# Optimization experiments

Measured on AMD Instinct MI355X. Metric: run time of the kernel, lower is better.

The kernel has to match this reference:

```python
import jax, jax.numpy as jnp
import numpy as np

N, E, D_IN, D, HEADS = 8192, 2048, 256, 256, 4
EPS = 1e-5
NEG = -1e9  # large negative instead of -inf (rows guaranteed non-empty anyway)


def _layernorm(x, g, b):
    mu = jnp.mean(x, axis=-1, keepdims=True)
    var = jnp.mean(jnp.square(x - mu), axis=-1, keepdims=True)
    return (x - mu) * jax.lax.rsqrt(var + EPS) * g + b


def _mha(q_x, kv_x, in_w, in_b, out_w, out_b, mask):
    """torch nn.MultiheadAttention (batch=1, eval) with boolean attn_mask.
    q_x: [Lq, D], kv_x: [Lk, D], mask: [Lq, Lk] True = blocked."""
    hd = D // HEADS
    wq, wk, wv = jnp.split(in_w, 3, axis=0)   # each [D, D]
    bq, bk, bv = jnp.split(in_b, 3, axis=0)
    q = (q_x @ wq.T + bq).reshape(-1, HEADS, hd).transpose(1, 0, 2)  # [h, Lq, hd]
    k = (kv_x @ wk.T + bk).reshape(-1, HEADS, hd).transpose(1, 0, 2)
    v = (kv_x @ wv.T + bv).reshape(-1, HEADS, hd).transpose(1, 0, 2)
    scores = jnp.einsum('hqd,hkd->hqk', q, k) / jnp.sqrt(jnp.asarray(hd, q.dtype))
    scores = jnp.where(mask[None, :, :], NEG, scores)
    attn = jax.nn.softmax(scores, axis=-1)
    out = jnp.einsum('hqk,hkd->hqd', attn, v)           # [h, Lq, hd]
    out = out.transpose(1, 0, 2).reshape(-1, D)          # [Lq, D]
    return out @ out_w.T + out_b


def setup_inputs() -> dict:
    key = jax.random.key(0)
    ks = jax.random.split(key, 12)
    s = 0.02
    x_0 = jax.random.normal(ks[0], (N, D_IN), jnp.float32)
    x_1 = jax.random.normal(ks[1], (E, D_IN), jnp.float32)
    H = (jax.random.uniform(ks[2], (N, E)) < 0.01).astype(jnp.float32)
    H = H.at[jnp.arange(N), jnp.arange(N) % E].set(1.0)
    return {
        'x_0': x_0, 'x_1': x_1, 'incidence_1': H,
        'node_w': jax.random.normal(ks[3], (D, D_IN), jnp.float32) * s,
        'node_b': jnp.zeros((D,), jnp.float32),
        'edge_w': jax.random.normal(ks[4], (D, D_IN), jnp.float32) * s,
        'edge_b': jnp.zeros((D,), jnp.float32),
        'n2e_in_w': jax.random.normal(ks[5], (3 * D, D), jnp.float32) * s,
        'n2e_in_b': jnp.zeros((3 * D,), jnp.float32),
        'n2e_out_w': jax.random.normal(ks[6], (D, D), jnp.float32) * s,
        'n2e_out_b': jnp.zeros((D,), jnp.float32),
        'e2n_in_w': jax.random.normal(ks[7], (3 * D, D), jnp.float32) * s,
        'e2n_in_b': jnp.zeros((3 * D,), jnp.float32),
        'e2n_out_w': jax.random.normal(ks[8], (D, D), jnp.float32) * s,
        'e2n_out_b': jnp.zeros((D,), jnp.float32),
        'norm1_g': jnp.ones((D,), jnp.float32),
        'norm1_b': jnp.zeros((D,), jnp.float32),
        'norm2_g': jnp.ones((D,), jnp.float32),
        'norm2_b': jnp.zeros((D,), jnp.float32),
    }


def reference(x_0, x_1, incidence_1, node_w, node_b, edge_w, edge_b,
              n2e_in_w, n2e_in_b, n2e_out_w, n2e_out_b,
              e2n_in_w, e2n_in_b, e2n_out_w, e2n_out_b,
              norm1_g, norm1_b, norm2_g, norm2_b):
    H = incidence_1                      # [N, E]
    x_0_p = x_0 @ node_w.T + node_b      # [N, D]
    x_1_p = x_1 @ edge_w.T + edge_b      # [E, D]
    # node -> edge: edges query nodes, mask where H.T == 0
    x_1_u = _mha(x_1_p, x_0_p, n2e_in_w, n2e_in_b, n2e_out_w, n2e_out_b,
                 H.T == 0)
    x_1_u = _layernorm(x_1_p + x_1_u, norm1_g, norm1_b)
    # edge -> node: nodes query updated edges, mask where H == 0
    x_0_u = _mha(x_0_p, x_1_u, e2n_in_w, e2n_in_b, e2n_out_w, e2n_out_b,
                 H == 0)
    x_0_u = _layernorm(x_0_p + x_0_u, norm2_g, norm2_b)
    return (x_0_u, x_1_u)
```

## Files before the change

kernel.cpp:

```cpp
#include <hip/hip_runtime.h>
#include <hip/hip_bf16.h>

using bf16 = __hip_bfloat16;
typedef __attribute__((ext_vector_type(4))) float  f32x4;
typedef __attribute__((ext_vector_type(8))) short  s16x8;

#define QSTRIDE 1040
#define ASTRIDE 520
#define BSTRIDE 2064
#define CMAX 256
#define RMAX 128

struct ConvDesc { const float* src[14]; int dstoff[14]; int cnt[14]; };

__global__ __launch_bounds__(256)
void conv_weights(ConvDesc d, bf16* __restrict__ dst, int* __restrict__ cz, int czn)
{
    const int seg = blockIdx.x >> 6;
    const int blk = blockIdx.x & 63;
    if (seg == 14) {
        for (int i = blk * 256 + threadIdx.x; i < czn; i += 64 * 256)
            cz[i] = 0;
        return;
    }
    const float* __restrict__ s = d.src[seg];
    bf16* __restrict__ o = dst + d.dstoff[seg];
    const int n = d.cnt[seg];
    for (int i = blk * 256 + threadIdx.x; i < n; i += 64 * 256)
        o[i] = __float2bfloat16(s[i]);
}

__global__ __launch_bounds__(256, 2)
void build_proj(const float* __restrict__ H, int* __restrict__ col_cnt,
                unsigned short* __restrict__ col_idx, int* __restrict__ row_cnt,
                unsigned short* __restrict__ row_idx,
                const float* __restrict__ X0, const float* __restrict__ X1,
                const bf16* __restrict__ Wc, const bf16* __restrict__ biasc,
                bf16* __restrict__ outB)
{
    __shared__ __align__(16) char smem[8 * QSTRIDE * 2];
    const int t = threadIdx.x;

    if (blockIdx.x < 8192) {
        int* rc = (int*)smem;
        const int n = blockIdx.x;
        if (t == 0) *rc = 0;
        __syncthreads();

        const float* Hp = H + (size_t)n * 2048 + t * 8;
        f32x4 h0 = *(const f32x4*)Hp;
        f32x4 h1 = *(const f32x4*)(Hp + 4);
        float hv[8];
#pragma unroll
        for (int j = 0; j < 4; j++) { hv[j] = h0[j]; hv[4 + j] = h1[j]; }

#pragma unroll
        for (int j = 0; j < 8; j++) {
            if (hv[j] != 0.f) {
                const int e = t * 8 + j;
                const int sr = atomicAdd(rc, 1);
                if (sr < RMAX) row_idx[(size_t)n * RMAX + sr] = (unsigned short)e;
                const int sc = atomicAdd(&col_cnt[e], 1);
                if (sc < CMAX) col_idx[(size_t)e * CMAX + sc] = (unsigned short)n;
            }
        }
        __syncthreads();
        if (t == 0) row_cnt[n] = (*rc < RMAX) ? *rc : RMAX;
        return;
    }

    bf16* As = (bf16*)smem;
    bf16* Bs = As + 4 * QSTRIDE;

    const int lane = t & 63;
    const int w    = t >> 6;
    const int wm   = (w >> 1) * 64;
    const int wn   = (w & 1) * 64;
    const int pb   = blockIdx.x - 8192;
    const int bt   = pb >> 1;
    const int tn   = (pb & 1) * 128;

    const float* __restrict__ A = (bt < 64) ? X0 : X1;
    const int arow = (bt < 64) ? bt * 128 : (bt - 64) * 128;
    const bf16* __restrict__ W    = Wc    + ((bt < 64) ? 0 : 65536);
    const bf16* __restrict__ bias = biasc + ((bt < 64) ? 0 : 256);
    const int tm = bt * 128;

    f32x4 acc[4][4];
#pragma unroll
    for (int i = 0; i < 4; i++)
#pragma unroll
        for (int j = 0; j < 4; j++)
#pragma unroll
            for (int r = 0; r < 4; r++) acc[i][j][r] = 0.f;

    const int m0 = t >> 2,         q0 = t & 3;
    const int m1 = (t + 256) >> 2, q1 = (t + 256) & 3;
    const int fq = lane >> 4, fr = lane & 15;

    for (int k0 = 0; k0 < 256; k0 += 32) {
        f32x4 a0l = *(const f32x4*)(A + (size_t)(arow + m0) * 256 + k0 + q0 * 8);
        f32x4 a0h = *(const f32x4*)(A + (size_t)(arow + m0) * 256 + k0 + q0 * 8 + 4);
        f32x4 a1l = *(const f32x4*)(A + (size_t)(arow + m1) * 256 + k0 + q1 * 8);
        f32x4 a1h = *(const f32x4*)(A + (size_t)(arow + m1) * 256 + k0 + q1 * 8 + 4);
        union { s16x8 v; bf16 e[8]; } u0, u1;
#pragma unroll
        for (int j = 0; j < 4; j++) {
            u0.e[j] = __float2bfloat16(a0l[j]); u0.e[4 + j] = __float2bfloat16(a0h[j]);
            u1.e[j] = __float2bfloat16(a1l[j]); u1.e[4 + j] = __float2bfloat16(a1h[j]);
        }
        s16x8 sb0 = *(const s16x8*)(W + (size_t)(tn + m0) * 256 + k0 + q0 * 8);
        s16x8 sb1 = *(const s16x8*)(W + (size_t)(tn + m1) * 256 + k0 + q1 * 8);

        __syncthreads();
        *(s16x8*)&As[q0 * QSTRIDE + m0 * 8] = u0.v;
        *(s16x8*)&As[q1 * QSTRIDE + m1 * 8] = u1.v;
        *(s16x8*)&Bs[q0 * QSTRIDE + m0 * 8] = sb0;
        *(s16x8*)&Bs[q1 * QSTRIDE + m1 * 8] = sb1;
        __syncthreads();

        s16x8 af[4], bfv[4];
#pragma unroll
        for (int i = 0; i < 4; i++) {
            af[i]  = *(const s16x8*)&As[fq * QSTRIDE + (wm + i * 16 + fr) * 8];
            bfv[i] = *(const s16x8*)&Bs[fq * QSTRIDE + (wn + i * 16 + fr) * 8];
        }
#pragma unroll
        for (int i = 0; i < 4; i++)
#pragma unroll
            for (int j = 0; j < 4; j++)
                acc[i][j] = __builtin_amdgcn_mfma_f32_16x16x32_bf16(
                    af[i], bfv[j], acc[i][j], 0, 0, 0);
    }

#pragma unroll
    for (int j = 0; j < 4; j++) {
        const int ncol = tn + wn + j * 16 + fr;
        const float bj = __bfloat162float(bias[ncol]);
#pragma unroll
        for (int i = 0; i < 4; i++)
#pragma unroll
            for (int r = 0; r < 4; r++) {
                const int mrow = tm + wm + i * 16 + fq * 4 + r;
                outB[(size_t)mrow * 256 + ncol] = __float2bfloat16(acc[i][j][r] + bj);
            }
    }
}

__global__ __launch_bounds__(256, 2)
void gemm_dual(const bf16* __restrict__ A0, const bf16* __restrict__ W0,
               const bf16* __restrict__ bias0, bf16* __restrict__ out0,
               int N0, int tiles0, int nblk0,
               const bf16* __restrict__ A1, const bf16* __restrict__ W1,
               const bf16* __restrict__ bias1, bf16* __restrict__ out1,
               int N1, int tiles1)
{
    __shared__ __align__(16) bf16 As[4 * QSTRIDE];
    __shared__ __align__(16) bf16 Bs[4 * QSTRIDE];

    const int t    = threadIdx.x;
    const int lane = t & 63;
    const int w    = t >> 6;
    const int wm   = (w >> 1) * 64;
    const int wn   = (w & 1) * 64;

    const bool second = (blockIdx.x >= (unsigned)nblk0);
    const int  bi     = second ? (blockIdx.x - nblk0) : blockIdx.x;
    const bf16* __restrict__ A    = second ? A1 : A0;
    const bf16* __restrict__ W    = second ? W1 : W0;
    const bf16* __restrict__ bias = second ? bias1 : bias0;
    bf16* __restrict__ outB       = second ? out1 : out0;
    const int N      = second ? N1 : N0;
    const int tilesN = second ? tiles1 : tiles0;
    const int tm = (bi / tilesN) * 128;
    const int tn = (bi % tilesN) * 128;

    f32x4 acc[4][4];
#pragma unroll
    for (int i = 0; i < 4; i++)
#pragma unroll
        for (int j = 0; j < 4; j++)
#pragma unroll
            for (int r = 0; r < 4; r++) acc[i][j][r] = 0.f;

    const int m0 = t >> 2,         q0 = t & 3;
    const int m1 = (t + 256) >> 2, q1 = (t + 256) & 3;
    const int fq = lane >> 4, fr = lane & 15;

    for (int k0 = 0; k0 < 256; k0 += 32) {
        s16x8 sa0 = *(const s16x8*)(A + (size_t)(tm + m0) * 256 + k0 + q0 * 8);
        s16x8 sa1 = *(const s16x8*)(A + (size_t)(tm + m1) * 256 + k0 + q1 * 8);
        s16x8 sb0 = *(const s16x8*)(W + (size_t)(tn + m0) * 256 + k0 + q0 * 8);
        s16x8 sb1 = *(const s16x8*)(W + (size_t)(tn + m1) * 256 + k0 + q1 * 8);

        __syncthreads();
        *(s16x8*)&As[q0 * QSTRIDE + m0 * 8] = sa0;
        *(s16x8*)&As[q1 * QSTRIDE + m1 * 8] = sa1;
        *(s16x8*)&Bs[q0 * QSTRIDE + m0 * 8] = sb0;
        *(s16x8*)&Bs[q1 * QSTRIDE + m1 * 8] = sb1;
        __syncthreads();

        s16x8 af[4], bfv[4];
#pragma unroll
        for (int i = 0; i < 4; i++) {
            af[i]  = *(const s16x8*)&As[fq * QSTRIDE + (wm + i * 16 + fr) * 8];
            bfv[i] = *(const s16x8*)&Bs[fq * QSTRIDE + (wn + i * 16 + fr) * 8];
        }
#pragma unroll
        for (int i = 0; i < 4; i++)
#pragma unroll
            for (int j = 0; j < 4; j++)
                acc[i][j] = __builtin_amdgcn_mfma_f32_16x16x32_bf16(
                    af[i], bfv[j], acc[i][j], 0, 0, 0);
    }

#pragma unroll
    for (int j = 0; j < 4; j++) {
        const int ncol = tn + wn + j * 16 + fr;
        const float bj = __bfloat162float(bias[ncol]);
#pragma unroll
        for (int i = 0; i < 4; i++)
#pragma unroll
            for (int r = 0; r < 4; r++) {
                const int mrow = tm + wm + i * 16 + fq * 4 + r;
                outB[(size_t)mrow * N + ncol] = __float2bfloat16(acc[i][j][r] + bj);
            }
    }
}

__global__ __launch_bounds__(256, 2)
void gemm_ln(const bf16* __restrict__ A, const bf16* __restrict__ W,
             const float* __restrict__ biasF, const bf16* __restrict__ xp,
             const float* __restrict__ g, const float* __restrict__ b,
             float* __restrict__ outF, bf16* __restrict__ outB)
{
    __shared__ __align__(16) bf16 As[4 * ASTRIDE];
    __shared__ __align__(16) bf16 Bs[4 * BSTRIDE];
    __shared__ float rs1[64], rs2[64];

    const int t    = threadIdx.x;
    const int lane = t & 63;
    const int w    = t >> 6;
    const int fq   = lane >> 4;
    const int fr   = lane & 15;
    const int tm   = blockIdx.x * 64;

    if (t < 64) { rs1[t] = 0.f; rs2[t] = 0.f; }

    f32x4 acc[4][4];
#pragma unroll
    for (int i = 0; i < 4; i++)
#pragma unroll
        for (int j = 0; j < 4; j++)
#pragma unroll
            for (int r = 0; r < 4; r++) acc[i][j][r] = 0.f;

    const int mA = t >> 2, qA = t & 3;

    for (int k0 = 0; k0 < 256; k0 += 32) {
        s16x8 sa = *(const s16x8*)(A + (size_t)(tm + mA) * 256 + k0 + qA * 8);
        s16x8 sb[4];
#pragma unroll
        for (int s = 0; s < 4; s++)
            sb[s] = *(const s16x8*)(W + (size_t)(mA + 64 * s) * 256 + k0 + qA * 8);

        __syncthreads();
        *(s16x8*)&As[qA * ASTRIDE + mA * 8] = sa;
#pragma unroll
        for (int s = 0; s < 4; s++)
            *(s16x8*)&Bs[qA * BSTRIDE + (mA + 64 * s) * 8] = sb[s];
        __syncthreads();

        s16x8 af[4], bfv[4];
#pragma unroll
        for (int i = 0; i < 4; i++) {
            af[i]  = *(const s16x8*)&As[fq * ASTRIDE + (i * 16 + fr) * 8];
            bfv[i] = *(const s16x8*)&Bs[fq * BSTRIDE + (w * 64 + i * 16 + fr) * 8];
        }
#pragma unroll
        for (int i = 0; i < 4; i++)
#pragma unroll
            for (int j = 0; j < 4; j++)
                acc[i][j] = __builtin_amdgcn_mfma_f32_16x16x32_bf16(
                    af[i], bfv[j], acc[i][j], 0, 0, 0);
    }

    float bj[4], gj[4], bbj[4];
    int colv[4];
#pragma unroll
    for (int j = 0; j < 4; j++) {
        colv[j] = w * 64 + j * 16 + fr;
        bj[j]  = biasF[colv[j]];
        gj[j]  = g[colv[j]];
        bbj[j] = b[colv[j]];
    }

#pragma unroll
    for (int i = 0; i < 4; i++) {
#pragma unroll
        for (int r = 0; r < 4; r++) {
            const int row = i * 16 + fq * 4 + r;
            float t1 = 0.f, t2 = 0.f;
#pragma unroll
            for (int j = 0; j < 4; j++) {
                float v = acc[i][j][r] + bj[j]
                        + __bfloat162float(xp[(size_t)(tm + row) * 256 + colv[j]]);
                acc[i][j][r] = v;
                t1 += v;
                t2 += v * v;
            }
#pragma unroll
            for (int o = 1; o < 16; o <<= 1) {
                t1 += __shfl_xor(t1, o);
                t2 += __shfl_xor(t2, o);
            }
            if (fr == 0) {
                atomicAdd(&rs1[row], t1);
                atomicAdd(&rs2[row], t2);
            }
        }
    }
    __syncthreads();

#pragma unroll
    for (int i = 0; i < 4; i++) {
#pragma unroll
        for (int r = 0; r < 4; r++) {
            const int row = i * 16 + fq * 4 + r;
            const float mu  = rs1[row] * (1.f / 256.f);
            const float var = rs2[row] * (1.f / 256.f) - mu * mu;
            const float rstd = rsqrtf(var + 1e-5f);
#pragma unroll
            for (int j = 0; j < 4; j++) {
                const float y = (acc[i][j][r] - mu) * rstd * gj[j] + bbj[j];
                outF[(size_t)(tm + row) * 256 + colv[j]] = y;
                if (outB) outB[(size_t)(tm + row) * 256 + colv[j]] = __float2bfloat16(y);
            }
        }
    }
}

__global__ __launch_bounds__(256)
void sparse_attn(const bf16* __restrict__ Q, int qs,
                 const bf16* __restrict__ Kb, const bf16* __restrict__ Vb, int kvs,
                 const int* __restrict__ cnts, const unsigned short* __restrict__ idx,
                 int lmax, int idxmask, bf16* __restrict__ out)
{
    __shared__ float sc[4][CMAX];
    __shared__ unsigned short nls[CMAX];
    const int qi   = blockIdx.x;
    const int h    = threadIdx.x >> 6;
    const int lane = threadIdx.x & 63;
    const int grp  = lane >> 3;
    const int sub  = lane & 7;

    int n = cnts[qi];
    if (n > lmax) n = lmax;

    if (h == 0)
        for (int i = lane; i < n; i += 64)
            nls[i] = (unsigned short)(((int)idx[(size_t)qi * lmax + i]) & idxmask);
    __syncthreads();

    if (n <= 0) {
        out[(size_t)qi * 256 + h * 64 + lane] = __float2bfloat16(0.f);
        return;
    }

    float qv[8];
    {
        union { f32x4 v; unsigned short u[8]; } qu;
        qu.v = *(const f32x4*)(Q + (size_t)qi * qs + h * 64 + sub * 8);
#pragma unroll
        for (int j = 0; j < 8; j++)
            qv[j] = __uint_as_float(((unsigned)qu.u[j]) << 16) * 0.125f;
    }

    float mx = -1e30f;
#pragma unroll 2
    for (int base = 0; base < n; base += 8) {
        const int i = base + grp;
        float s = -1e30f;
        if (i < n) {
            const int nb = nls[i];
            union { f32x4 v; unsigned short u[8]; } ku;
            ku.v = *(const f32x4*)(Kb + (size_t)nb * kvs + h * 64 + sub * 8);
            float a = 0.f;
#pragma unroll
            for (int j = 0; j < 8; j++)
                a += __uint_as_float(((unsigned)ku.u[j]) << 16) * qv[j];
            a += __shfl_xor(a, 1);
            a += __shfl_xor(a, 2);
            a += __shfl_xor(a, 4);
            if (sub == 0) sc[h][i] = a;
            s = a;
        }
        mx = fmaxf(mx, s);
    }
#pragma unroll
    for (int o = 32; o > 0; o >>= 1) mx = fmaxf(mx, __shfl_xor(mx, o));

    float sum = 0.f;
    for (int base = 0; base < n; base += 64) {
        const int i = base + lane;
        if (i < n) {
            const float p = __expf(sc[h][i] - mx);
            sc[h][i] = p;
            sum += p;
        }
    }
#pragma unroll
    for (int o = 32; o > 0; o >>= 1) sum += __shfl_xor(sum, o);
    const float inv = 1.f / sum;

    float oa[8];
#pragma unroll
    for (int j = 0; j < 8; j++) oa[j] = 0.f;
#pragma unroll 2
    for (int base = 0; base < n; base += 8) {
        const int i = base + grp;
        if (i < n) {
            const float p = sc[h][i];
            const int nb = nls[i];
            union { f32x4 v; unsigned short u[8]; } vu;
            vu.v = *(const f32x4*)(Vb + (size_t)nb * kvs + h * 64 + sub * 8);
#pragma unroll
            for (int j = 0; j < 8; j++)
                oa[j] += p * __uint_as_float(((unsigned)vu.u[j]) << 16);
        }
    }
#pragma unroll
    for (int j = 0; j < 8; j++) {
        oa[j] += __shfl_xor(oa[j], 8);
        oa[j] += __shfl_xor(oa[j], 16);
        oa[j] += __shfl_xor(oa[j], 32);
    }
    if (grp == 0) {
        union { s16x8 v; bf16 e[8]; } ou;
#pragma unroll
        for (int j = 0; j < 8; j++) ou.e[j] = __float2bfloat16(oa[j] * inv);
        *(s16x8*)(out + (size_t)qi * 256 + h * 64 + sub * 8) = ou.v;
    }
}

extern "C" void kernel_launch(void* const* d_in, const int* in_sizes, int n_in,
                              void* d_out, int out_size, void* d_ws, size_t ws_size,
                              hipStream_t stream)
{
    const int N = 8192, E = 2048;

    float* out0 = (float*)d_out;
    float* out1 = (float*)d_out + (size_t)N * 256;

    char* wp = (char*)d_ws;
    auto carve = [&](size_t bytes) { void* p = wp; wp += (bytes + 15) & ~size_t(15); return p; };

    bf16*  wcat    = (bf16*)          carve(657408 * 2);
    int*   col_cnt = (int*)           carve((size_t)E * 4);
    int*   row_cnt = (int*)           carve((size_t)N * 4);
    unsigned short* col_idx = (unsigned short*)carve((size_t)E * CMAX * 2);
    unsigned short* row_idx = (unsigned short*)carve((size_t)N * RMAX * 2);
    bf16*  xp01    = (bf16*) carve((size_t)(N + E) * 256 * 2);
    bf16*  kvq     = (bf16*) carve((size_t)N * 768 * 2);
    bf16*  q1      = (bf16*) carve((size_t)E * 256 * 2);
    bf16*  attn1   = (bf16*) carve((size_t)E * 256 * 2);
    bf16*  x1u_b   = (bf16*) carve((size_t)E * 256 * 2);
    bf16*  kv2     = (bf16*) carve((size_t)E * 512 * 2);
    bf16*  attn2   = (bf16*) carve((size_t)N * 256 * 2);

    bf16* x0p = xp01;
    bf16* x1p = xp01 + (size_t)N * 256;

    const int O_PW   = 0;
    const int O_PB   = 131072;
    const int O_KVQ  = 131584;
    const int O_KVQB = 328192;
    const int O_Q1W  = 328960;
    const int O_Q1B  = 394496;
    const int O_KV2W = 394752;
    const int O_KV2B = 525824;
    const int O_O1W  = 526336;
    const int O_O2W  = 591872;

    ConvDesc cd;
    const float* srcs[14] = {
        (const float*)d_in[3], (const float*)d_in[5],
        (const float*)d_in[4], (const float*)d_in[6],
        (const float*)d_in[7] + 65536, (const float*)d_in[11],
        (const float*)d_in[8] + 256,   (const float*)d_in[12],
        (const float*)d_in[7],         (const float*)d_in[8],
        (const float*)d_in[11] + 65536,(const float*)d_in[12] + 256,
        (const float*)d_in[9],         (const float*)d_in[13]
    };
    const int offs[14] = {O_PW, O_PW + 65536, O_PB, O_PB + 256,
                          O_KVQ, O_KVQ + 131072, O_KVQB, O_KVQB + 512,
                          O_Q1W, O_Q1B, O_KV2W, O_KV2B, O_O1W, O_O2W};
    const int cnts[14] = {65536, 65536, 256, 256, 131072, 65536, 512, 256,
                          65536, 256, 131072, 512, 65536, 65536};
    for (int i = 0; i < 14; i++) { cd.src[i] = srcs[i]; cd.dstoff[i] = offs[i]; cd.cnt[i] = cnts[i]; }

    conv_weights<<<15 * 64, 256, 0, stream>>>(cd, wcat, col_cnt, E);

    build_proj<<<8192 + 160, 256, 0, stream>>>((const float*)d_in[2], col_cnt,
                                               col_idx, row_cnt, row_idx,
                                               (const float*)d_in[0], (const float*)d_in[1],
                                               wcat + O_PW, wcat + O_PB, xp01);

    gemm_dual<<<384 + 32, 256, 0, stream>>>(x0p, wcat + O_KVQ, wcat + O_KVQB, kvq,
                                            768, 6, 384,
                                            x1p, wcat + O_Q1W, wcat + O_Q1B, q1,
                                            256, 2);

    sparse_attn<<<E, 256, 0, stream>>>(q1, 256, kvq, kvq + 256, 768,
                                       col_cnt, col_idx, CMAX, N - 1, attn1);
    gemm_ln<<<E / 64, 256, 0, stream>>>(attn1, wcat + O_O1W, (const float*)d_in[10],
                                        x1p, (const float*)d_in[15], (const float*)d_in[16],
                                        out1, x1u_b);

    gemm_dual<<<64, 256, 0, stream>>>(x1u_b, wcat + O_KV2W, wcat + O_KV2B, kv2,
                                      512, 4, 64,
                                      nullptr, nullptr, nullptr, nullptr, 256, 2);
    sparse_attn<<<N, 256, 0, stream>>>(kvq + 512, 768, kv2, kv2 + 256, 512,
                                       row_cnt, row_idx, RMAX, E - 1, attn2);
    gemm_ln<<<N / 64, 256, 0, stream>>>(attn2, wcat + O_O2W, (const float*)d_in[14],
                                        x0p, (const float*)d_in[17], (const float*)d_in[18],
                                        out0, nullptr);
}
```

Before: 273.2 us.

## Split incidence-list building from projection GEMM into persistent prefetching kernel

Separates the fused build_proj kernel into a build_lists kernel and a gemm_proj kernel. The list builder now uses 1024 persistent blocks that each loop over 8 rows of H and prefetch the next row while processing the current one. It also needs only a small LDS footprint, where before every row block carried the GEMM's large shared allocation. The aim is better occupancy and latency hiding when scanning the dense incidence matrix. The cost is one extra kernel launch, and the projection GEMM no longer overlaps with the list building.

```diff
diff --git a/kernel.cpp b/kernel.cpp
--- a/kernel.cpp
+++ b/kernel.cpp
@@ -30,55 +30,68 @@
         o[i] = __float2bfloat16(s[i]);
 }
 
-__global__ __launch_bounds__(256, 2)
-void build_proj(const float* __restrict__ H, int* __restrict__ col_cnt,
-                unsigned short* __restrict__ col_idx, int* __restrict__ row_cnt,
-                unsigned short* __restrict__ row_idx,
-                const float* __restrict__ X0, const float* __restrict__ X1,
-                const bf16* __restrict__ Wc, const bf16* __restrict__ biasc,
-                bf16* __restrict__ outB)
-{
-    __shared__ __align__(16) char smem[8 * QSTRIDE * 2];
+__global__ __launch_bounds__(256)
+void build_lists(const float* __restrict__ H, int* __restrict__ col_cnt,
+                 unsigned short* __restrict__ col_idx, int* __restrict__ row_cnt,
+                 unsigned short* __restrict__ row_idx)
+{
+    __shared__ int rc;
     const int t = threadIdx.x;
 
-    if (blockIdx.x < 8192) {
-        int* rc = (int*)smem;
-        const int n = blockIdx.x;
-        if (t == 0) *rc = 0;
-        __syncthreads();
-
-        const float* Hp = H + (size_t)n * 2048 + t * 8;
-        f32x4 h0 = *(const f32x4*)Hp;
-        f32x4 h1 = *(const f32x4*)(Hp + 4);
+    int n = blockIdx.x;
+    const float* Hp = H + (size_t)n * 2048 + t * 8;
+    f32x4 c0 = *(const f32x4*)Hp;
+    f32x4 c1 = *(const f32x4*)(Hp + 4);
+
+    while (n < 8192) {
+        const int nn = n + 1024;
+        f32x4 p0, p1;
+        if (nn < 8192) {
+            const float* Hq = H + (size_t)nn * 2048 + t * 8;
+            p0 = *(const f32x4*)Hq;
+            p1 = *(const f32x4*)(Hq + 4);
+        }
+
+        if (t == 0) rc = 0;
+        __syncthreads();
+
         float hv[8];
 #pragma unroll
-        for (int j = 0; j < 4; j++) { hv[j] = h0[j]; hv[4 + j] = h1[j]; }
+        for (int j = 0; j < 4; j++) { hv[j] = c0[j]; hv[4 + j] = c1[j]; }
 
 #pragma unroll
         for (int j = 0; j < 8; j++) {
             if (hv[j] != 0.f) {
                 const int e = t * 8 + j;
-                const int sr = atomicAdd(rc, 1);
+                const int sr = atomicAdd(&rc, 1);
                 if (sr < RMAX) row_idx[(size_t)n * RMAX + sr] = (unsigned short)e;
                 const int sc = atomicAdd(&col_cnt[e], 1);
                 if (sc < CMAX) col_idx[(size_t)e * CMAX + sc] = (unsigned short)n;
             }
         }
         __syncthreads();
-        if (t == 0) row_cnt[n] = (*rc < RMAX) ? *rc : RMAX;
-        return;
-    }
-
-    bf16* As = (bf16*)smem;
-    bf16* Bs = As + 4 * QSTRIDE;
-
+        if (t == 0) row_cnt[n] = (rc < RMAX) ? rc : RMAX;
+
+        n = nn; c0 = p0; c1 = p1;
+    }
+}
+
+__global__ __launch_bounds__(256, 2)
+void gemm_proj(const float* __restrict__ X0, const float* __restrict__ X1,
+               const bf16* __restrict__ Wc, const bf16* __restrict__ biasc,
+               bf16* __restrict__ outB)
+{
+    __shared__ __align__(16) bf16 As[4 * QSTRIDE];
+    __shared__ __align__(16) bf16 Bs[4 * QSTRIDE];
+
+    const int t    = threadIdx.x;
     const int lane = t & 63;
     const int w    = t >> 6;
     const int wm   = (w >> 1) * 64;
     const int wn   = (w & 1) * 64;
-    const int pb   = blockIdx.x - 8192;
-    const int bt   = pb >> 1;
-    const int tn   = (pb & 1) * 128;
+    const int bt   = blockIdx.x >> 1;
+    const int tn   = (blockIdx.x & 1) * 128;
+    if (bt >= 80) return;
 
     const float* __restrict__ A = (bt < 64) ? X0 : X1;
     const int arow = (bt < 64) ? bt * 128 : (bt - 64) * 128;
@@ -501,10 +514,11 @@
 
     conv_weights<<<15 * 64, 256, 0, stream>>>(cd, wcat, col_cnt, E);
 
-    build_proj<<<8192 + 160, 256, 0, stream>>>((const float*)d_in[2], col_cnt,
-                                               col_idx, row_cnt, row_idx,
-                                               (const float*)d_in[0], (const float*)d_in[1],
-                                               wcat + O_PW, wcat + O_PB, xp01);
+    build_lists<<<1024, 256, 0, stream>>>((const float*)d_in[2], col_cnt, col_idx,
+                                          row_cnt, row_idx);
+
+    gemm_proj<<<160, 256, 0, stream>>>((const float*)d_in[0], (const float*)d_in[1],
+                                       wcat + O_PW, wcat + O_PB, xp01);
 
     gemm_dual<<<384 + 32, 256, 0, stream>>>(x0p, wcat + O_KVQ, wcat + O_KVQB, kvq,
                                             768, 6, 384,
```

Measured after the change: 270.2 us (median of 2 runs). Within noise of the previous version (-1.1%).
